# Performance work log

Measured on AMD Instinct MI355X. Metric: run time of the kernel, lower is better.

The kernel has to match this reference:

```python
import jax, jax.numpy as jnp
import numpy as np

G, N_NODES, E, H, D, IN_DIM, NS = 1024, 64, 128, 8, 32, 256, 48
EPS = 1e-6

def setup_inputs() -> dict:
    key = jax.random.key(0)
    ks = jax.random.split(key, 10)
    s = 1.0 / np.sqrt(IN_DIM)
    return {
        'h': jax.random.normal(ks[0], (G * N_NODES, IN_DIM), jnp.float32),
        'Wq': jax.random.normal(ks[1], (IN_DIM, H * D), jnp.float32) * s,
        'bq': jax.random.normal(ks[2], (H * D,), jnp.float32) * 0.01,
        'Wk': jax.random.normal(ks[3], (IN_DIM, H * D), jnp.float32) * s,
        'bk': jax.random.normal(ks[4], (H * D,), jnp.float32) * 0.01,
        'Wv': jax.random.normal(ks[5], (IN_DIM, H * D), jnp.float32) * s,
        'bv': jax.random.normal(ks[6], (H * D,), jnp.float32) * 0.01,
        'src': jax.random.randint(ks[7], (E,), 0, N_NODES, jnp.int32),
        'dst': jax.random.randint(ks[8], (E,), 0, N_NODES, jnp.int32),
        'ns': jax.random.randint(ks[9], (E, NS), 0, N_NODES, jnp.int32),
    }

def reference(h, Wq, bq, Wk, bk, Wv, bv, src, dst, ns):
    # per-node projections, reshaped per-graph: [G, n, H, D]
    Q = (h @ Wq + bq).reshape(G, N_NODES, H, D)
    K = (h @ Wk + bk).reshape(G, N_NODES, H, D)
    V = (h @ Wv + bv).reshape(G, N_NODES, H, D)
    # QK[g, s, h, t] = Q[g,s,h] . K[g,t,h], clamped as in torch .clamp(-5, 5)
    QK = jnp.clip(jnp.einsum('gshd,gthd->gsht', Q, K), -5.0, 5.0)  # [G, n, H, n]
    QKs = QK[:, src]  # rows for each edge's source node: [G, E, H, n]
    # numerator: QK[:, src_e, :, dst_e]
    num = jnp.take_along_axis(
        QKs, jnp.broadcast_to(dst[None, :, None, None].astype(jnp.int32), (G, E, H, 1)), axis=3
    )[..., 0]  # [G, E, H]
    # denominator: sum of QK[:, src_e, :, non_siblings(e)]
    den = jnp.take_along_axis(
        QKs, jnp.broadcast_to(ns[None, :, None, :], (G, E, H, NS)), axis=3
    ).sum(-1)  # [G, E, H]
    score = num / (den + EPS)  # [G, E, H]
    # scatter-sum aggregation: wV[g, dst] += V[g, src] * score; z[g, dst] += score
    msg = V[:, src] * score[..., None]  # [G, E, H, D]
    seg = (jnp.arange(G, dtype=jnp.int32)[:, None] * N_NODES + dst[None, :]).reshape(-1)
    wV = jax.ops.segment_sum(msg.reshape(G * E, H, D), seg, num_segments=G * N_NODES)
    z = jax.ops.segment_sum(score.reshape(G * E, H), seg, num_segments=G * N_NODES)
    return wV / (z[..., None] + EPS)  # [G*n, H, D]
```

## Files before the change

kernel.cpp:

```cpp
#include <hip/hip_runtime.h>

#define NG    1024
#define NN    64
#define NE    128
#define NH    8
#define ND    32
#define INDIM 256
#define NS_   48
#define EPS_  1e-6
#define BK    16

#define GBM   128
#define GBN   64
#define GBK   64

#define WS_QKV_FLOATS ((size_t)NG * NH * 3 * NN * ND)
#define WS_ELIST_OFF  (WS_QKV_FLOATS * sizeof(float))
#define WS_CNT_OFF    (WS_ELIST_OFF + (size_t)NN * 64 * sizeof(unsigned short))
#define WS_NEED2      (WS_CNT_OFF + (size_t)NN * sizeof(int))

typedef _Float16 half8_t __attribute__((ext_vector_type(8)));
typedef _Float16 half4_t __attribute__((ext_vector_type(4)));
typedef float    f32x4_t __attribute__((ext_vector_type(4)));

__device__ __forceinline__ void async_ld16(const float* gp, float* lp) {
  __builtin_amdgcn_global_load_lds(
      (const __attribute__((address_space(1))) void*)gp,
      (__attribute__((address_space(3))) void*)lp, 16, 0, 0);
}

__global__ __launch_bounds__(256, 2) void qkv_gemm_kernel(
    const float* __restrict__ h,
    const float* __restrict__ Wq, const float* __restrict__ bq,
    const float* __restrict__ Wk, const float* __restrict__ bk,
    float* __restrict__ ws)
{
  const int b    = blockIdx.x;
  const int xcd  = b & 7;
  const int slot = b >> 3;
  const int rt   = xcd * 128 + (slot >> 2);
  const int sel  = (slot >> 1) & 1;
  const int ct   = slot & 1;
  const int tid  = threadIdx.x;

  const float* W  = (sel == 0) ? Wq : Wk;
  const float* bs = (sel == 0) ? bq : bk;

  __shared__ __align__(16) float hT[2][64][16];
  __shared__ __align__(16) float wT[2][16][128];

  const int ty  = tid >> 5;
  const int tx  = tid & 31;
  const int r8  = ty * 8;
  const int ca  = tx * 4;

  const int wvid = tid >> 6;
  const int lane = tid & 63;

  float acc[8][4];
  #pragma unroll
  for (int i = 0; i < 8; ++i)
    #pragma unroll
    for (int j = 0; j < 4; ++j) acc[i][j] = 0.f;

  const float* gA = h + ((size_t)(rt * 64 + wvid * 16 + (lane >> 2))) * INDIM
                      + (lane & 3) * 4;
  const float* gB0 = W + ((size_t)(wvid * 4 + 0 + (lane >> 5))) * (NH * ND)
                       + ct * 128 + (lane & 31) * 4;
  const float* gB1 = W + ((size_t)(wvid * 4 + 2 + (lane >> 5))) * (NH * ND)
                       + ct * 128 + (lane & 31) * 4;
  float* lA[2]  = { &hT[0][wvid * 16][0], &hT[1][wvid * 16][0] };
  float* lB0[2] = { &wT[0][wvid * 4 + 0][0], &wT[1][wvid * 4 + 0][0] };
  float* lB1[2] = { &wT[0][wvid * 4 + 2][0], &wT[1][wvid * 4 + 2][0] };

  async_ld16(gA, lA[0]);
  async_ld16(gB0, lB0[0]);
  async_ld16(gB1, lB1[0]);

  for (int kc = 0; kc < INDIM / BK; ++kc) {
    __syncthreads();

    if (kc + 1 < INDIM / BK) {
      const int k0n = (kc + 1) * BK;
      const int nb  = (kc + 1) & 1;
      async_ld16(gA + k0n, lA[nb]);
      async_ld16(gB0 + (size_t)k0n * (NH * ND), lB0[nb]);
      async_ld16(gB1 + (size_t)k0n * (NH * ND), lB1[nb]);
    }

    const int cb = kc & 1;
    #pragma unroll
    for (int kg = 0; kg < 4; ++kg) {
      f32x4_t a4[8];
      #pragma unroll
      for (int i = 0; i < 8; ++i)
        a4[i] = *(const f32x4_t*)&hT[cb][r8 + i][kg * 4];
      f32x4_t b4[4];
      #pragma unroll
      for (int kk = 0; kk < 4; ++kk)
        b4[kk] = *(const f32x4_t*)&wT[cb][kg * 4 + kk][ca];

      #pragma unroll
      for (int kk = 0; kk < 4; ++kk) {
        const f32x4_t bb = b4[kk];
        #pragma unroll
        for (int i = 0; i < 8; ++i) {
          const float ai = a4[i][kk];
          acc[i][0] += ai * bb[0];
          acc[i][1] += ai * bb[1];
          acc[i][2] += ai * bb[2];
          acc[i][3] += ai * bb[3];
        }
      }
    }
  }

  const int col = ct * 128 + ca;
  const int hda = col >> 5, d0a = col & 31;
  float ba4[4];
  #pragma unroll
  for (int j = 0; j < 4; ++j) ba4[j] = bs[col + j];

  #pragma unroll
  for (int i = 0; i < 8; ++i) {
    const int r = rt * 64 + r8 + i;
    const int g = r >> 6, n = r & 63;
    float* opa = ws + ((((size_t)(g * NH + hda)) * 3 + sel) * NN + n) * ND + d0a;
    *(float4*)opa = make_float4(acc[i][0] + ba4[0], acc[i][1] + ba4[1],
                                acc[i][2] + ba4[2], acc[i][3] + ba4[3]);
  }
}

__device__ __forceinline__ void* swz_pt(void* base, int row, int k) {
  size_t byte = ((size_t)(row * GBK + k)) * 2;
  byte ^= (size_t)((row & 7) << 4);
  return (void*)((char*)base + byte);
}

__global__ __launch_bounds__(256, 2) void v_gemm_mfma(
    const float* __restrict__ h,
    const float* __restrict__ Wv, const float* __restrict__ bv,
    const int* __restrict__ dst,
    unsigned short* __restrict__ elist, int* __restrict__ cnt,
    float* __restrict__ ws)
{
  const int b = blockIdx.x;
  if (b >= 2048) {
    const int n = threadIdx.x;
    if (n < NN) {
      int c = 0;
      for (int e = 0; e < NE; ++e) {
        if (dst[e] == n) {
          if (c < 64) elist[n * 64 + c] = (unsigned short)e;
          ++c;
        }
      }
      cnt[n] = (c > 64) ? 64 : c;
    }
    return;
  }

  const int xcd  = b & 7;
  const int slot = b >> 3;
  const int rt   = xcd * 64 + (slot >> 2);
  const int ct   = slot & 3;

  __shared__ __align__(16) _Float16 Ahh[GBM * GBK];
  __shared__ __align__(16) _Float16 Ahl[GBM * GBK];
  __shared__ __align__(16) _Float16 Bhh[GBN * GBK];
  __shared__ __align__(16) _Float16 Bhl[GBN * GBK];

  const int tid  = threadIdx.x;
  const int lane = tid & 63;
  const int wvid = tid >> 6;
  const int wm   = wvid >> 1;
  const int wn   = wvid & 1;
  const int lr   = lane & 15;
  const int lg   = lane >> 4;

  f32x4_t acc0[4][2], acc1[4][2];
  #pragma unroll
  for (int i = 0; i < 4; ++i)
    #pragma unroll
    for (int j = 0; j < 2; ++j) {
      acc0[i][j] = (f32x4_t){0.f, 0.f, 0.f, 0.f};
      acc1[i][j] = (f32x4_t){0.f, 0.f, 0.f, 0.f};
    }

  const float* hA  = h + (size_t)rt * GBM * INDIM;
  const int bnn    = tid >> 2;
  const int bkh    = (tid & 3) * 16;
  const int c0     = ct * GBN;
  const float* wB  = Wv + (size_t)bkh * (NH * ND) + (c0 + bnn);

  for (int kc = 0; kc < INDIM / GBK; ++kc) {
    float4 av4[8];
    #pragma unroll
    for (int i = 0; i < 8; ++i) {
      const int idx = i * 256 + tid;
      const int row = idx >> 4, kq = idx & 15;
      av4[i] = *(const float4*)(hA + (size_t)row * INDIM + kc * GBK + kq * 4);
    }
    float wv16[16];
    #pragma unroll
    for (int j = 0; j < 16; ++j)
      wv16[j] = wB[(size_t)(kc * GBK + j) * (NH * ND)];

    if (kc) __syncthreads();

    #pragma unroll
    for (int i = 0; i < 8; ++i) {
      const int idx = i * 256 + tid;
      const int row = idx >> 4, kq = idx & 15;
      half4_t ph, pl;
      ph[0] = (_Float16)av4[i].x; ph[1] = (_Float16)av4[i].y;
      ph[2] = (_Float16)av4[i].z; ph[3] = (_Float16)av4[i].w;
      pl[0] = (_Float16)((av4[i].x - (float)ph[0]) * 2048.f);
      pl[1] = (_Float16)((av4[i].y - (float)ph[1]) * 2048.f);
      pl[2] = (_Float16)((av4[i].z - (float)ph[2]) * 2048.f);
      pl[3] = (_Float16)((av4[i].w - (float)ph[3]) * 2048.f);
      *(half4_t*)swz_pt(Ahh, row, kq * 4) = ph;
      *(half4_t*)swz_pt(Ahl, row, kq * 4) = pl;
    }
    #pragma unroll
    for (int c = 0; c < 2; ++c) {
      half8_t ph, pl;
      #pragma unroll
      for (int j = 0; j < 8; ++j) {
        const float a  = wv16[c * 8 + j];
        const _Float16 x = (_Float16)a;
        ph[j] = x;
        pl[j] = (_Float16)((a - (float)x) * 2048.f);
      }
      *(half8_t*)swz_pt(Bhh, bnn, bkh + c * 8) = ph;
      *(half8_t*)swz_pt(Bhl, bnn, bkh + c * 8) = pl;
    }
    __syncthreads();

    #pragma unroll
    for (int ks = 0; ks < 2; ++ks) {
      const int kb = ks * 32 + lg * 8;
      half8_t bh[2], bl[2];
      #pragma unroll
      for (int j = 0; j < 2; ++j) {
        const int colr = wn * 32 + j * 16 + lr;
        bh[j] = *(const half8_t*)swz_pt(Bhh, colr, kb);
        bl[j] = *(const half8_t*)swz_pt(Bhl, colr, kb);
      }
      #pragma unroll
      for (int i = 0; i < 4; ++i) {
        const int rowr = wm * 64 + i * 16 + lr;
        const half8_t ah = *(const half8_t*)swz_pt(Ahh, rowr, kb);
        const half8_t al = *(const half8_t*)swz_pt(Ahl, rowr, kb);
        #pragma unroll
        for (int j = 0; j < 2; ++j) {
          acc0[i][j] = __builtin_amdgcn_mfma_f32_16x16x32_f16(
              ah, bh[j], acc0[i][j], 0, 0, 0);
          acc1[i][j] = __builtin_amdgcn_mfma_f32_16x16x32_f16(
              ah, bl[j], acc1[i][j], 0, 0, 0);
          acc1[i][j] = __builtin_amdgcn_mfma_f32_16x16x32_f16(
              al, bh[j], acc1[i][j], 0, 0, 0);
        }
      }
    }
  }

  float bj[2];
  #pragma unroll
  for (int j = 0; j < 2; ++j) bj[j] = bv[c0 + wn * 32 + j * 16 + lr];

  #pragma unroll
  for (int i = 0; i < 4; ++i) {
    #pragma unroll
    for (int r = 0; r < 4; ++r) {
      const int R = rt * GBM + wm * 64 + i * 16 + lg * 4 + r;
      const int g = R >> 6, n = R & 63;
      #pragma unroll
      for (int j = 0; j < 2; ++j) {
        const int col = c0 + wn * 32 + j * 16 + lr;
        const int hd = col >> 5, d = col & 31;
        const float val = acc0[i][j][r] + acc1[i][j][r] * (1.0f / 2048.0f)
                          + bj[j];
        ws[((((size_t)(g * NH + hd)) * 3 + 2) * NN + n) * ND + d] = val;
      }
    }
  }
}

#define QSW(k, c) ((c) ^ ((((k) >> 3) & 3) << 2))

__global__ __launch_bounds__(256, 5) void attn_kernel(
    const float* __restrict__ ws,
    const int* __restrict__ src, const int* __restrict__ dst,
    const int* __restrict__ ns,
    const unsigned short* __restrict__ elist_g, const int* __restrict__ cnt_g,
    float* __restrict__ out, const int g0)
{
  const int hd  = blockIdx.x;
  const int g   = g0 + blockIdx.y;
  const int tid = threadIdx.x;
  const int ty  = tid >> 4, tx = tid & 15;

  __shared__ union {
    struct { float QT[32][68]; float KT[32][68]; } a;
    float QK[64][65];
  } uQ;
  __shared__ float Vs[64][36];
  __shared__ float  score_s[NE];
  __shared__ int    srcs[NE];
  __shared__ double z_s[NN];

  const float* base = ws + ((size_t)(g * NH + hd)) * 3 * (NN * ND);
  {
    const int nr = tid >> 3;
    const int d4 = (tid & 7) * 4;
    #pragma unroll
    for (int half = 0; half < 2; ++half) {
      const int n = half * 32 + nr;
      float4 q = *(const float4*)(base + (size_t)n * ND + d4);
      float4 k = *(const float4*)(base + (size_t)(NN * ND) + (size_t)n * ND + d4);
      float4 v = *(const float4*)(base + (size_t)(2 * NN * ND) + (size_t)n * ND + d4);
      uQ.a.QT[d4 + 0][QSW(d4 + 0, n)] = q.x;
      uQ.a.QT[d4 + 1][QSW(d4 + 1, n)] = q.y;
      uQ.a.QT[d4 + 2][QSW(d4 + 2, n)] = q.z;
      uQ.a.QT[d4 + 3][QSW(d4 + 3, n)] = q.w;
      uQ.a.KT[d4 + 0][QSW(d4 + 0, n)] = k.x;
      uQ.a.KT[d4 + 1][QSW(d4 + 1, n)] = k.y;
      uQ.a.KT[d4 + 2][QSW(d4 + 2, n)] = k.z;
      uQ.a.KT[d4 + 3][QSW(d4 + 3, n)] = k.w;
      *(float4*)&Vs[n][d4] = v;
    }
  }
  __syncthreads();

  {
    const int s0 = ty * 4, t0 = tx * 4;
    float qk[4][4];
    #pragma unroll
    for (int i = 0; i < 4; ++i)
      #pragma unroll
      for (int j = 0; j < 4; ++j) qk[i][j] = 0.f;
    #pragma unroll
    for (int k = 0; k < ND; ++k) {
      float4 qa = *(const float4*)&uQ.a.QT[k][QSW(k, s0)];
      float4 kb = *(const float4*)&uQ.a.KT[k][QSW(k, t0)];
      qk[0][0] += qa.x * kb.x; qk[0][1] += qa.x * kb.y; qk[0][2] += qa.x * kb.z; qk[0][3] += qa.x * kb.w;
      qk[1][0] += qa.y * kb.x; qk[1][1] += qa.y * kb.y; qk[1][2] += qa.y * kb.z; qk[1][3] += qa.y * kb.w;
      qk[2][0] += qa.z * kb.x; qk[2][1] += qa.z * kb.y; qk[2][2] += qa.z * kb.z; qk[2][3] += qa.z * kb.w;
      qk[3][0] += qa.w * kb.x; qk[3][1] += qa.w * kb.y; qk[3][2] += qa.w * kb.z; qk[3][3] += qa.w * kb.w;
    }
    __syncthreads();
    #pragma unroll
    for (int i = 0; i < 4; ++i)
      #pragma unroll
      for (int j = 0; j < 4; ++j) {
        float v = qk[i][j];
        v = fminf(5.f, fmaxf(-5.f, v));
        uQ.QK[s0 + i][t0 + j] = v;
      }
  }
  __syncthreads();

  if (tid < NE) {
    const int e = tid;
    const int s = src[e];
    srcs[e] = s;
    const float num = uQ.QK[s][dst[e]];
    double den = 0.0;
    const int* np_ = ns + (size_t)e * NS_;
    #pragma unroll
    for (int j = 0; j < NS_; ++j) den += (double)uQ.QK[s][np_[j]];
    score_s[e] = (float)((double)num / (den + (double)EPS_));
  }
  __syncthreads();

  if (tid < NN) {
    const int cn = cnt_g[tid];
    double zz = 0.0;
    for (int c = 0; c < cn; ++c)
      zz += (double)score_s[elist_g[tid * 64 + c]];
    z_s[tid] = zz;
  }
  __syncthreads();

  {
    const int n  = tid >> 2;
    const int d0 = (tid & 3) * 8;
    float wvv[8];
    #pragma unroll
    for (int i = 0; i < 8; ++i) wvv[i] = 0.f;
    const int cn = cnt_g[n];
    for (int c = 0; c < cn; ++c) {
      const int e  = elist_g[n * 64 + c];
      const float sc = score_s[e];
      const int s  = srcs[e];
      float4 v0 = *(const float4*)&Vs[s][d0];
      float4 v1 = *(const float4*)&Vs[s][d0 + 4];
      wvv[0] += sc * v0.x; wvv[1] += sc * v0.y; wvv[2] += sc * v0.z; wvv[3] += sc * v0.w;
      wvv[4] += sc * v1.x; wvv[5] += sc * v1.y; wvv[6] += sc * v1.z; wvv[7] += sc * v1.w;
    }
    const double zz = z_s[n] + (double)EPS_;
    float o[8];
    #pragma unroll
    for (int i = 0; i < 8; ++i) o[i] = (float)((double)wvv[i] / zz);
    float* op = out + (((size_t)(g * NN + n)) * NH + hd) * ND + d0;
    *(float4*)(op)     = make_float4(o[0], o[1], o[2], o[3]);
    *(float4*)(op + 4) = make_float4(o[4], o[5], o[6], o[7]);
  }
}

__global__ __launch_bounds__(256, 4) void raal_fused_kernel(
    const float* __restrict__ h,
    const float* __restrict__ Wq, const float* __restrict__ bq,
    const float* __restrict__ Wk, const float* __restrict__ bk,
    const float* __restrict__ Wv, const float* __restrict__ bv,
    const int*   __restrict__ src, const int* __restrict__ dst,
    const int*   __restrict__ ns,
    float* __restrict__ out)
{
  const int hd  = blockIdx.x;
  const int g   = blockIdx.y;
  const int tid = threadIdx.x;
  const int ty  = tid >> 4, tx = tid & 15;

  __shared__ union {
    struct { float QT[32][64]; float KT[32][64]; } s2;
    float QK[64][64];
  } uQ;
  __shared__ float Vs[64][32];
  __shared__ union {
    struct { float hT[BK][68]; float wT[BK][100]; } s1;
    struct { float score[NE]; int srcs[NE]; int dsts[NE];
             double z[NN]; unsigned short elist[NN][64]; int cnt[NN]; } s3;
  } uA;

  const int r0 = ty * 4;
  const int c4 = tx * 4;
  const int cv = tx * 2;

  float accqk[4][4], accv[4][2];
  #pragma unroll
  for (int i = 0; i < 4; ++i) {
    #pragma unroll
    for (int j = 0; j < 4; ++j) accqk[i][j] = 0.f;
    accv[i][0] = 0.f; accv[i][1] = 0.f;
  }

  const int lr  = tid >> 2;
  const int lk4 = (tid & 3) * 4;
  const int wr  = ty;
  const int wc  = tx * 2;
  const float* hrow = h + ((size_t)(g * NN + lr)) * INDIM + lk4;
  const size_t wcol = (size_t)hd * ND + wc;

  float4 hv; float2 wq2, wk2, wv2;
  {
    hv  = *(const float4*)(hrow);
    const size_t wro = (size_t)wr * (NH * ND) + wcol;
    wq2 = *(const float2*)(Wq + wro);
    wk2 = *(const float2*)(Wk + wro);
    wv2 = *(const float2*)(Wv + wro);
  }

  for (int kc = 0; kc < INDIM / BK; ++kc) {
    __syncthreads();
    uA.s1.hT[lk4 + 0][lr] = hv.x;
    uA.s1.hT[lk4 + 1][lr] = hv.y;
    uA.s1.hT[lk4 + 2][lr] = hv.z;
    uA.s1.hT[lk4 + 3][lr] = hv.w;
    *(float2*)&uA.s1.wT[wr][ 0 + wc] = wq2;
    *(float2*)&uA.s1.wT[wr][32 + wc] = wk2;
    *(float2*)&uA.s1.wT[wr][64 + wc] = wv2;
    __syncthreads();

    if (kc + 1 < INDIM / BK) {
      const int k0n = (kc + 1) * BK;
      hv  = *(const float4*)(hrow + k0n);
      const size_t wro = (size_t)(k0n + wr) * (NH * ND) + wcol;
      wq2 = *(const float2*)(Wq + wro);
      wk2 = *(const float2*)(Wk + wro);
      wv2 = *(const float2*)(Wv + wro);
    }

    #pragma unroll
    for (int k = 0; k < BK; ++k) {
      float4 a  = *(const float4*)&uA.s1.hT[k][r0];
      float4 b  = *(const float4*)&uA.s1.wT[k][c4];
      float2 bv2 = *(const float2*)&uA.s1.wT[k][64 + cv];
      #pragma unroll
      for (int i = 0; i < 4; ++i) {
        const float ai = (i == 0) ? a.x : (i == 1) ? a.y : (i == 2) ? a.z : a.w;
        accqk[i][0] += ai * b.x;
        accqk[i][1] += ai * b.y;
        accqk[i][2] += ai * b.z;
        accqk[i][3] += ai * b.w;
        accv[i][0]  += ai * bv2.x;
        accv[i][1]  += ai * bv2.y;
      }
    }
  }

  {
    if (tx < 8) {
      #pragma unroll
      for (int j = 0; j < 4; ++j) {
        const int c = c4 + j;
        const float b = bq[hd * ND + c];
        #pragma unroll
        for (int i = 0; i < 4; ++i) uQ.s2.QT[c][r0 + i] = accqk[i][j] + b;
      }
    } else {
      #pragma unroll
      for (int j = 0; j < 4; ++j) {
        const int c = c4 - 32 + j;
        const float b = bk[hd * ND + c];
        #pragma unroll
        for (int i = 0; i < 4; ++i) uQ.s2.KT[c][r0 + i] = accqk[i][j] + b;
      }
    }
    const float b0 = bv[hd * ND + cv], b1 = bv[hd * ND + cv + 1];
    #pragma unroll
    for (int i = 0; i < 4; ++i) {
      Vs[r0 + i][cv]     = accv[i][0] + b0;
      Vs[r0 + i][cv + 1] = accv[i][1] + b1;
    }
  }
  __syncthreads();

  {
    const int s0 = ty * 4, t0 = tx * 4;
    float qk[4][4];
    #pragma unroll
    for (int i = 0; i < 4; ++i)
      #pragma unroll
      for (int j = 0; j < 4; ++j) qk[i][j] = 0.f;
    #pragma unroll
    for (int k = 0; k < ND; ++k) {
      float4 qa = *(const float4*)&uQ.s2.QT[k][s0];
      float4 kb = *(const float4*)&uQ.s2.KT[k][t0];
      qk[0][0] += qa.x * kb.x; qk[0][1] += qa.x * kb.y; qk[0][2] += qa.x * kb.z; qk[0][3] += qa.x * kb.w;
      qk[1][0] += qa.y * kb.x; qk[1][1] += qa.y * kb.y; qk[1][2] += qa.y * kb.z; qk[1][3] += qa.y * kb.w;
      qk[2][0] += qa.z * kb.x; qk[2][1] += qa.z * kb.y; qk[2][2] += qa.z * kb.z; qk[2][3] += qa.z * kb.w;
      qk[3][0] += qa.w * kb.x; qk[3][1] += qa.w * kb.y; qk[3][2] += qa.w * kb.z; qk[3][3] += qa.w * kb.w;
    }
    __syncthreads();
    #pragma unroll
    for (int i = 0; i < 4; ++i)
      #pragma unroll
      for (int j = 0; j < 4; ++j) {
        float v = qk[i][j];
        v = fminf(5.f, fmaxf(-5.f, v));
        uQ.QK[s0 + i][t0 + j] = v;
      }
  }
  __syncthreads();

  if (tid < NE) {
    const int e = tid;
    const int s = src[e], dd = dst[e];
    uA.s3.srcs[e] = s; uA.s3.dsts[e] = dd;
    const float num = uQ.QK[s][dd];
    double den = 0.0;
    const int* np_ = ns + (size_t)e * NS_;
    #pragma unroll
    for (int j = 0; j < NS_; ++j) den += (double)uQ.QK[s][np_[j]];
    uA.s3.score[e] = (float)((double)num / (den + (double)EPS_));
  }
  __syncthreads();

  if (tid < NN) {
    int c = 0; double zz = 0.0;
    for (int e = 0; e < NE; ++e) {
      if (uA.s3.dsts[e] == tid) {
        zz += (double)uA.s3.score[e];
        if (c < 64) uA.s3.elist[tid][c] = (unsigned short)e;
        ++c;
      }
    }
    uA.s3.cnt[tid] = (c > 64) ? 64 : c;
    uA.s3.z[tid]   = zz;
  }
  __syncthreads();

  {
    const int n  = tid >> 2;
    const int d0 = (tid & 3) * 8;
    float wvv[8];
    #pragma unroll
    for (int i = 0; i < 8; ++i) wvv[i] = 0.f;
    const int cn = uA.s3.cnt[n];
    for (int c = 0; c < cn; ++c) {
      const int e  = uA.s3.elist[n][c];
      const float sc = uA.s3.score[e];
      const int s  = uA.s3.srcs[e];
      float4 v0 = *(const float4*)&Vs[s][d0];
      float4 v1 = *(const float4*)&Vs[s][d0 + 4];
      wvv[0] += sc * v0.x; wvv[1] += sc * v0.y; wvv[2] += sc * v0.z; wvv[3] += sc * v0.w;
      wvv[4] += sc * v1.x; wvv[5] += sc * v1.y; wvv[6] += sc * v1.z; wvv[7] += sc * v1.w;
    }
    const double zz = uA.s3.z[n] + (double)EPS_;
    float o[8];
    #pragma unroll
    for (int i = 0; i < 8; ++i) o[i] = (float)((double)wvv[i] / zz);
    float* op = out + (((size_t)(g * NN + n)) * NH + hd) * ND + d0;
    *(float4*)(op)     = make_float4(o[0], o[1], o[2], o[3]);
    *(float4*)(op + 4) = make_float4(o[4], o[5], o[6], o[7]);
  }
}

extern "C" void kernel_launch(void* const* d_in, const int* in_sizes, int n_in,
                              void* d_out, int out_size, void* d_ws, size_t ws_size,
                              hipStream_t stream) {
  const float* h   = (const float*)d_in[0];
  const float* Wq  = (const float*)d_in[1];
  const float* bq  = (const float*)d_in[2];
  const float* Wk  = (const float*)d_in[3];
  const float* bk  = (const float*)d_in[4];
  const float* Wv  = (const float*)d_in[5];
  const float* bv  = (const float*)d_in[6];
  const int*   src = (const int*)d_in[7];
  const int*   dst = (const int*)d_in[8];
  const int*   ns  = (const int*)d_in[9];
  float* out = (float*)d_out;

  dim3 b(256, 1, 1);
  if (ws_size >= WS_NEED2) {
    float* ws = (float*)d_ws;
    unsigned short* elist = (unsigned short*)((char*)d_ws + WS_ELIST_OFF);
    int* cnt = (int*)((char*)d_ws + WS_CNT_OFF);

    hipLaunchKernelGGL(qkv_gemm_kernel, dim3(4096, 1, 1), b, 0, stream,
                       h, Wq, bq, Wk, bk, ws);
    hipLaunchKernelGGL(v_gemm_mfma, dim3(2049, 1, 1), b, 0, stream,
                       h, Wv, bv, dst, elist, cnt, ws);
    hipLaunchKernelGGL(attn_kernel, dim3(NH, NG / 2, 1), b, 0, stream,
                       ws, src, dst, ns, elist, cnt, out, 0);
    hipLaunchKernelGGL(attn_kernel, dim3(NH, NG / 2, 1), b, 0, stream,
                       ws, src, dst, ns, elist, cnt, out, NG / 2);
  } else {
    hipLaunchKernelGGL(raal_fused_kernel, dim3(NH, NG, 1), b, 0, stream,
                       h, Wq, bq, Wk, bk, Wv, bv, src, dst, ns, out);
  }
}
```

Measured before the change: 461.7 us.

## Merge QK and V projection GEMMs into one launch and single attention launch

Combines the FP32 Q/K projection kernel and the split-FP16 MFMA V projection kernel into one grid, interleaving two QK blocks with one V block per triple and sharing LDS through a union. The two half-grid attention launches are collapsed into one full-grid launch. This removes launch overhead and the tail gaps between kernels, and lets the compute-heavy MFMA blocks overlap with the FMA-based blocks. The cost is register and LDS pressure set by the larger of the two paths, which may lower occupancy for the QK blocks.

```diff
diff --git a/kernel.cpp b/kernel.cpp
--- a/kernel.cpp
+++ b/kernel.cpp
@@ -29,124 +29,32 @@
       (__attribute__((address_space(3))) void*)lp, 16, 0, 0);
 }
 
-__global__ __launch_bounds__(256, 2) void qkv_gemm_kernel(
-    const float* __restrict__ h,
-    const float* __restrict__ Wq, const float* __restrict__ bq,
-    const float* __restrict__ Wk, const float* __restrict__ bk,
-    float* __restrict__ ws)
-{
-  const int b    = blockIdx.x;
-  const int xcd  = b & 7;
-  const int slot = b >> 3;
-  const int rt   = xcd * 128 + (slot >> 2);
-  const int sel  = (slot >> 1) & 1;
-  const int ct   = slot & 1;
-  const int tid  = threadIdx.x;
-
-  const float* W  = (sel == 0) ? Wq : Wk;
-  const float* bs = (sel == 0) ? bq : bk;
-
-  __shared__ __align__(16) float hT[2][64][16];
-  __shared__ __align__(16) float wT[2][16][128];
-
-  const int ty  = tid >> 5;
-  const int tx  = tid & 31;
-  const int r8  = ty * 8;
-  const int ca  = tx * 4;
-
-  const int wvid = tid >> 6;
-  const int lane = tid & 63;
-
-  float acc[8][4];
-  #pragma unroll
-  for (int i = 0; i < 8; ++i)
-    #pragma unroll
-    for (int j = 0; j < 4; ++j) acc[i][j] = 0.f;
-
-  const float* gA = h + ((size_t)(rt * 64 + wvid * 16 + (lane >> 2))) * INDIM
-                      + (lane & 3) * 4;
-  const float* gB0 = W + ((size_t)(wvid * 4 + 0 + (lane >> 5))) * (NH * ND)
-                       + ct * 128 + (lane & 31) * 4;
-  const float* gB1 = W + ((size_t)(wvid * 4 + 2 + (lane >> 5))) * (NH * ND)
-                       + ct * 128 + (lane & 31) * 4;
-  float* lA[2]  = { &hT[0][wvid * 16][0], &hT[1][wvid * 16][0] };
-  float* lB0[2] = { &wT[0][wvid * 4 + 0][0], &wT[1][wvid * 4 + 0][0] };
-  float* lB1[2] = { &wT[0][wvid * 4 + 2][0], &wT[1][wvid * 4 + 2][0] };
-
-  async_ld16(gA, lA[0]);
-  async_ld16(gB0, lB0[0]);
-  async_ld16(gB1, lB1[0]);
-
-  for (int kc = 0; kc < INDIM / BK; ++kc) {
-    __syncthreads();
-
-    if (kc + 1 < INDIM / BK) {
-      const int k0n = (kc + 1) * BK;
-      const int nb  = (kc + 1) & 1;
-      async_ld16(gA + k0n, lA[nb]);
-      async_ld16(gB0 + (size_t)k0n * (NH * ND), lB0[nb]);
-      async_ld16(gB1 + (size_t)k0n * (NH * ND), lB1[nb]);
-    }
-
-    const int cb = kc & 1;
-    #pragma unroll
-    for (int kg = 0; kg < 4; ++kg) {
-      f32x4_t a4[8];
-      #pragma unroll
-      for (int i = 0; i < 8; ++i)
-        a4[i] = *(const f32x4_t*)&hT[cb][r8 + i][kg * 4];
-      f32x4_t b4[4];
-      #pragma unroll
-      for (int kk = 0; kk < 4; ++kk)
-        b4[kk] = *(const f32x4_t*)&wT[cb][kg * 4 + kk][ca];
-
-      #pragma unroll
-      for (int kk = 0; kk < 4; ++kk) {
-        const f32x4_t bb = b4[kk];
-        #pragma unroll
-        for (int i = 0; i < 8; ++i) {
-          const float ai = a4[i][kk];
-          acc[i][0] += ai * bb[0];
-          acc[i][1] += ai * bb[1];
-          acc[i][2] += ai * bb[2];
-          acc[i][3] += ai * bb[3];
-        }
-      }
-    }
-  }
-
-  const int col = ct * 128 + ca;
-  const int hda = col >> 5, d0a = col & 31;
-  float ba4[4];
-  #pragma unroll
-  for (int j = 0; j < 4; ++j) ba4[j] = bs[col + j];
-
-  #pragma unroll
-  for (int i = 0; i < 8; ++i) {
-    const int r = rt * 64 + r8 + i;
-    const int g = r >> 6, n = r & 63;
-    float* opa = ws + ((((size_t)(g * NH + hda)) * 3 + sel) * NN + n) * ND + d0a;
-    *(float4*)opa = make_float4(acc[i][0] + ba4[0], acc[i][1] + ba4[1],
-                                acc[i][2] + ba4[2], acc[i][3] + ba4[3]);
-  }
-}
-
 __device__ __forceinline__ void* swz_pt(void* base, int row, int k) {
   size_t byte = ((size_t)(row * GBK + k)) * 2;
   byte ^= (size_t)((row & 7) << 4);
   return (void*)((char*)base + byte);
 }
 
-__global__ __launch_bounds__(256, 2) void v_gemm_mfma(
+__global__ __launch_bounds__(256, 2) void qkv_v_fused_kernel(
     const float* __restrict__ h,
+    const float* __restrict__ Wq, const float* __restrict__ bq,
+    const float* __restrict__ Wk, const float* __restrict__ bk,
     const float* __restrict__ Wv, const float* __restrict__ bv,
     const int* __restrict__ dst,
     unsigned short* __restrict__ elist, int* __restrict__ cnt,
     float* __restrict__ ws)
 {
-  const int b = blockIdx.x;
-  if (b >= 2048) {
-    const int n = threadIdx.x;
+  __shared__ __align__(16) union {
+    struct { float hT[2][64][16]; float wT[2][16][128]; } qk;
+    struct { _Float16 Ahh[GBM * GBK]; _Float16 Ahl[GBM * GBK];
+             _Float16 Bhh[GBN * GBK]; _Float16 Bhl[GBN * GBK]; } v;
+  } sm;
+
+  const int bid = blockIdx.x;
+  const int tid = threadIdx.x;
+
+  if (bid >= 6144) {
+    const int n = tid;
     if (n < NN) {
       int c = 0;
       for (int e = 0; e < NE; ++e) {
@@ -160,128 +68,216 @@
     return;
   }
 
-  const int xcd  = b & 7;
-  const int slot = b >> 3;
-  const int rt   = xcd * 64 + (slot >> 2);
-  const int ct   = slot & 3;
-
-  __shared__ __align__(16) _Float16 Ahh[GBM * GBK];
-  __shared__ __align__(16) _Float16 Ahl[GBM * GBK];
-  __shared__ __align__(16) _Float16 Bhh[GBN * GBK];
-  __shared__ __align__(16) _Float16 Bhl[GBN * GBK];
-
-  const int tid  = threadIdx.x;
+  const int trip = bid / 3;
+  const int rr   = bid % 3;
+  const int wvid = tid >> 6;
   const int lane = tid & 63;
-  const int wvid = tid >> 6;
-  const int wm   = wvid >> 1;
-  const int wn   = wvid & 1;
-  const int lr   = lane & 15;
-  const int lg   = lane >> 4;
-
-  f32x4_t acc0[4][2], acc1[4][2];
-  #pragma unroll
-  for (int i = 0; i < 4; ++i)
-    #pragma unroll
-    for (int j = 0; j < 2; ++j) {
-      acc0[i][j] = (f32x4_t){0.f, 0.f, 0.f, 0.f};
-      acc1[i][j] = (f32x4_t){0.f, 0.f, 0.f, 0.f};
-    }
-
-  const float* hA  = h + (size_t)rt * GBM * INDIM;
-  const int bnn    = tid >> 2;
-  const int bkh    = (tid & 3) * 16;
-  const int c0     = ct * GBN;
-  const float* wB  = Wv + (size_t)bkh * (NH * ND) + (c0 + bnn);
-
-  for (int kc = 0; kc < INDIM / GBK; ++kc) {
-    float4 av4[8];
+
+  if (rr < 2) {
+    const int b    = trip * 2 + rr;
+    const int xcd  = b & 7;
+    const int slot = b >> 3;
+    const int rt   = xcd * 128 + (slot >> 2);
+    const int sel  = (slot >> 1) & 1;
+    const int ct   = slot & 1;
+
+    const float* W  = (sel == 0) ? Wq : Wk;
+    const float* bs = (sel == 0) ? bq : bk;
+
+    const int ty  = tid >> 5;
+    const int tx  = tid & 31;
+    const int r8  = ty * 8;
+    const int ca  = tx * 4;
+
+    float acc[8][4];
+    #pragma unroll
+    for (int i = 0; i < 8; ++i)
+      #pragma unroll
+      for (int j = 0; j < 4; ++j) acc[i][j] = 0.f;
+
+    const float* gA = h + ((size_t)(rt * 64 + wvid * 16 + (lane >> 2))) * INDIM
+                        + (lane & 3) * 4;
+    const float* gB0 = W + ((size_t)(wvid * 4 + 0 + (lane >> 5))) * (NH * ND)
+                         + ct * 128 + (lane & 31) * 4;
+    const float* gB1 = W + ((size_t)(wvid * 4 + 2 + (lane >> 5))) * (NH * ND)
+                         + ct * 128 + (lane & 31) * 4;
+    float* lA[2]  = { &sm.qk.hT[0][wvid * 16][0], &sm.qk.hT[1][wvid * 16][0] };
+    float* lB0[2] = { &sm.qk.wT[0][wvid * 4 + 0][0], &sm.qk.wT[1][wvid * 4 + 0][0] };
+    float* lB1[2] = { &sm.qk.wT[0][wvid * 4 + 2][0], &sm.qk.wT[1][wvid * 4 + 2][0] };
+
+    async_ld16(gA, lA[0]);
+    async_ld16(gB0, lB0[0]);
+    async_ld16(gB1, lB1[0]);
+
+    for (int kc = 0; kc < INDIM / BK; ++kc) {
+      __syncthreads();
+
+      if (kc + 1 < INDIM / BK) {
+        const int k0n = (kc + 1) * BK;
+        const int nb  = (kc + 1) & 1;
+        async_ld16(gA + k0n, lA[nb]);
+        async_ld16(gB0 + (size_t)k0n * (NH * ND), lB0[nb]);
+        async_ld16(gB1 + (size_t)k0n * (NH * ND), lB1[nb]);
+      }
+
+      const int cb = kc & 1;
+      #pragma unroll
+      for (int kg = 0; kg < 4; ++kg) {
+        f32x4_t a4[8];
+        #pragma unroll
+        for (int i = 0; i < 8; ++i)
+          a4[i] = *(const f32x4_t*)&sm.qk.hT[cb][r8 + i][kg * 4];
+        f32x4_t b4[4];
+        #pragma unroll
+        for (int kk = 0; kk < 4; ++kk)
+          b4[kk] = *(const f32x4_t*)&sm.qk.wT[cb][kg * 4 + kk][ca];
+
+        #pragma unroll
+        for (int kk = 0; kk < 4; ++kk) {
+          const f32x4_t bb = b4[kk];
+          #pragma unroll
+          for (int i = 0; i < 8; ++i) {
+            const float ai = a4[i][kk];
+            acc[i][0] = __builtin_fmaf(ai, bb[0], acc[i][0]);
+            acc[i][1] = __builtin_fmaf(ai, bb[1], acc[i][1]);
+            acc[i][2] = __builtin_fmaf(ai, bb[2], acc[i][2]);
+            acc[i][3] = __builtin_fmaf(ai, bb[3], acc[i][3]);
+          }
+        }
+      }
+    }
+
+    const int col = ct * 128 + ca;
+    const int hda = col >> 5, d0a = col & 31;
+    float ba4[4];
+    #pragma unroll
+    for (int j = 0; j < 4; ++j) ba4[j] = bs[col + j];
+
     #pragma unroll
     for (int i = 0; i < 8; ++i) {
-      const int idx = i * 256 + tid;
-      const int row = idx >> 4, kq = idx & 15;
-      av4[i] = *(const float4*)(hA + (size_t)row * INDIM + kc * GBK + kq * 4);
-    }
-    float wv16[16];
-    #pragma unroll
-    for (int j = 0; j < 16; ++j)
-      wv16[j] = wB[(size_t)(kc * GBK + j) * (NH * ND)];
-
-    if (kc) __syncthreads();
-
-    #pragma unroll
-    for (int i = 0; i < 8; ++i) {
-      const int idx = i * 256 + tid;
-      const int row = idx >> 4, kq = idx & 15;
-      half4_t ph, pl;
-      ph[0] = (_Float16)av4[i].x; ph[1] = (_Float16)av4[i].y;
-      ph[2] = (_Float16)av4[i].z; ph[3] = (_Float16)av4[i].w;
-      pl[0] = (_Float16)((av4[i].x - (float)ph[0]) * 2048.f);
-      pl[1] = (_Float16)((av4[i].y - (float)ph[1]) * 2048.f);
-      pl[2] = (_Float16)((av4[i].z - (float)ph[2]) * 2048.f);
-      pl[3] = (_Float16)((av4[i].w - (float)ph[3]) * 2048.f);
-      *(half4_t*)swz_pt(Ahh, row, kq * 4) = ph;
-      *(half4_t*)swz_pt(Ahl, row, kq * 4) = pl;
-    }
-    #pragma unroll
-    for (int c = 0; c < 2; ++c) {
-      half8_t ph, pl;
-      #pragma unroll
-      for (int j = 0; j < 8; ++j) {
-        const float a  = wv16[c * 8 + j];
-        const _Float16 x = (_Float16)a;
-        ph[j] = x;
-        pl[j] = (_Float16)((a - (float)x) * 2048.f);
-      }
-      *(half8_t*)swz_pt(Bhh, bnn, bkh + c * 8) = ph;
-      *(half8_t*)swz_pt(Bhl, bnn, bkh + c * 8) = pl;
-    }
-    __syncthreads();
-
-    #pragma unroll
-    for (int ks = 0; ks < 2; ++ks) {
-      const int kb = ks * 32 + lg * 8;
-      half8_t bh[2], bl[2];
+      const int r = rt * 64 + r8 + i;
+      const int g = r >> 6, n = r & 63;
+      float* opa = ws + ((((size_t)(g * NH + hda)) * 3 + sel) * NN + n) * ND + d0a;
+      *(float4*)opa = make_float4(acc[i][0] + ba4[0], acc[i][1] + ba4[1],
+                                  acc[i][2] + ba4[2], acc[i][3] + ba4[3]);
+    }
+  } else {
+    const int vb   = trip;
+    const int xcd  = vb & 7;
+    const int slot = vb >> 3;
+    const int rt   = xcd * 64 + (slot >> 2);
+    const int ct   = slot & 3;
+
+    const int wm   = wvid >> 1;
+    const int wn   = wvid & 1;
+    const int lr   = lane & 15;
+    const int lg   = lane >> 4;
+
+    f32x4_t acc0[4][2], acc1[4][2];
+    #pragma unroll
+    for (int i = 0; i < 4; ++i)
       #pragma unroll
       for (int j = 0; j < 2; ++j) {
-        const int colr = wn * 32 + j * 16 + lr;
-        bh[j] = *(const half8_t*)swz_pt(Bhh, colr, kb);
-        bl[j] = *(const half8_t*)swz_pt(Bhl, colr, kb);
-      }
-      #pragma unroll
-      for (int i = 0; i < 4; ++i) {
-        const int rowr = wm * 64 + i * 16 + lr;
-        const half8_t ah = *(const half8_t*)swz_pt(Ahh, rowr, kb);
-        const half8_t al = *(const half8_t*)swz_pt(Ahl, rowr, kb);
+        acc0[i][j] = (f32x4_t){0.f, 0.f, 0.f, 0.f};
+        acc1[i][j] = (f32x4_t){0.f, 0.f, 0.f, 0.f};
+      }
+
+    const float* hA  = h + (size_t)rt * GBM * INDIM;
+    const int bnn    = tid >> 2;
+    const int bkh    = (tid & 3) * 16;
+    const int c0     = ct * GBN;
+    const float* wB  = Wv + (size_t)bkh * (NH * ND) + (c0 + bnn);
+
+    for (int kc = 0; kc < INDIM / GBK; ++kc) {
+      float4 av4[8];
+      #pragma unroll
+      for (int i = 0; i < 8; ++i) {
+        const int idx = i * 256 + tid;
+        const int row = idx >> 4, kq = idx & 15;
+        av4[i] = *(const float4*)(hA + (size_t)row * INDIM + kc * GBK + kq * 4);
+      }
+      float wv16[16];
+      #pragma unroll
+      for (int j = 0; j < 16; ++j)
+        wv16[j] = wB[(size_t)(kc * GBK + j) * (NH * ND)];
+
+      if (kc) __syncthreads();
+
+      #pragma unroll
+      for (int i = 0; i < 8; ++i) {
+        const int idx = i * 256 + tid;
+        const int row = idx >> 4, kq = idx & 15;
+        half4_t ph, pl;
+        ph[0] = (_Float16)av4[i].x; ph[1] = (_Float16)av4[i].y;
+        ph[2] = (_Float16)av4[i].z; ph[3] = (_Float16)av4[i].w;
+        pl[0] = (_Float16)((av4[i].x - (float)ph[0]) * 2048.f);
+        pl[1] = (_Float16)((av4[i].y - (float)ph[1]) * 2048.f);
+        pl[2] = (_Float16)((av4[i].z - (float)ph[2]) * 2048.f);
+        pl[3] = (_Float16)((av4[i].w - (float)ph[3]) * 2048.f);
+        *(half4_t*)swz_pt(sm.v.Ahh, row, kq * 4) = ph;
+        *(half4_t*)swz_pt(sm.v.Ahl, row, kq * 4) = pl;
+      }
+      #pragma unroll
+      for (int c = 0; c < 2; ++c) {
+        half8_t ph, pl;
+        #pragma unroll
+        for (int j = 0; j < 8; ++j) {
+          const float a  = wv16[c * 8 + j];
+          const _Float16 x = (_Float16)a;
+          ph[j] = x;
+          pl[j] = (_Float16)((a - (float)x) * 2048.f);
+        }
+        *(half8_t*)swz_pt(sm.v.Bhh, bnn, bkh + c * 8) = ph;
+        *(half8_t*)swz_pt(sm.v.Bhl, bnn, bkh + c * 8) = pl;
+      }
+      __syncthreads();
+
+      #pragma unroll
+      for (int ks = 0; ks < 2; ++ks) {
+        const int kb = ks * 32 + lg * 8;
+        half8_t bh[2], bl[2];
         #pragma unroll
         for (int j = 0; j < 2; ++j) {
-          acc0[i][j] = __builtin_amdgcn_mfma_f32_16x16x32_f16(
-              ah, bh[j], acc0[i][j], 0, 0, 0);
-          acc1[i][j] = __builtin_amdgcn_mfma_f32_16x16x32_f16(
-              ah, bl[j], acc1[i][j], 0, 0, 0);
-          acc1[i][j] = __builtin_amdgcn_mfma_f32_16x16x32_f16(
-              al, bh[j], acc1[i][j], 0, 0, 0);
+          const int colr = wn * 32 + j * 16 + lr;
+          bh[j] = *(const half8_t*)swz_pt(sm.v.Bhh, colr, kb);
+          bl[j] = *(const half8_t*)swz_pt(sm.v.Bhl, colr, kb);
         }
-      }
-    }
-  }
-
-  float bj[2];
-  #pragma unroll
-  for (int j = 0; j < 2; ++j) bj[j] = bv[c0 + wn * 32 + j * 16 + lr];
-
-  #pragma unroll
-  for (int i = 0; i < 4; ++i) {
-    #pragma unroll
-    for (int r = 0; r < 4; ++r) {
-      const int R = rt * GBM + wm * 64 + i * 16 + lg * 4 + r;
-      const int g = R >> 6, n = R & 63;
-      #pragma unroll
-      for (int j = 0; j < 2; ++j) {
-        const int col = c0 + wn * 32 + j * 16 + lr;
-        const int hd = col >> 5, d = col & 31;
-        const float val = acc0[i][j][r] + acc1[i][j][r] * (1.0f / 2048.0f)
-                          + bj[j];
-        ws[((((size_t)(g * NH + hd)) * 3 + 2) * NN + n) * ND + d] = val;
+        #pragma unroll
+        for (int i = 0; i < 4; ++i) {
+          const int rowr = wm * 64 + i * 16 + lr;
+          const half8_t ah = *(const half8_t*)swz_pt(sm.v.Ahh, rowr, kb);
+          const half8_t al = *(const half8_t*)swz_pt(sm.v.Ahl, rowr, kb);
+          #pragma unroll
+          for (int j = 0; j < 2; ++j) {
+            acc0[i][j] = __builtin_amdgcn_mfma_f32_16x16x32_f16(
+                ah, bh[j], acc0[i][j], 0, 0, 0);
+            acc1[i][j] = __builtin_amdgcn_mfma_f32_16x16x32_f16(
+                ah, bl[j], acc1[i][j], 0, 0, 0);
+            acc1[i][j] = __builtin_amdgcn_mfma_f32_16x16x32_f16(
+                al, bh[j], acc1[i][j], 0, 0, 0);
+          }
+        }
+      }
+    }
+
+    float bj[2];
+    #pragma unroll
+    for (int j = 0; j < 2; ++j) bj[j] = bv[c0 + wn * 32 + j * 16 + lr];
+
+    #pragma unroll
+    for (int i = 0; i < 4; ++i) {
+      #pragma unroll
+      for (int r = 0; r < 4; ++r) {
+        const int R = rt * GBM + wm * 64 + i * 16 + lg * 4 + r;
+        const int g = R >> 6, n = R & 63;
+        #pragma unroll
+        for (int j = 0; j < 2; ++j) {
+          const int col = c0 + wn * 32 + j * 16 + lr;
+          const int hd = col >> 5, d = col & 31;
+          const float val = acc0[i][j][r] + acc1[i][j][r] * (1.0f / 2048.0f)
+                            + bj[j];
+          ws[((((size_t)(g * NH + hd)) * 3 + 2) * NN + n) * ND + d] = val;
+        }
       }
     }
   }
@@ -294,10 +290,10 @@
     const int* __restrict__ src, const int* __restrict__ dst,
     const int* __restrict__ ns,
     const unsigned short* __restrict__ elist_g, const int* __restrict__ cnt_g,
-    float* __restrict__ out, const int g0)
+    float* __restrict__ out)
 {
   const int hd  = blockIdx.x;
-  const int g   = g0 + blockIdx.y;
+  const int g   = blockIdx.y;
   const int tid = threadIdx.x;
   const int ty  = tid >> 4, tx = tid & 15;
 
@@ -629,14 +625,10 @@
     unsigned short* elist = (unsigned short*)((char*)d_ws + WS_ELIST_OFF);
     int* cnt = (int*)((char*)d_ws + WS_CNT_OFF);
 
-    hipLaunchKernelGGL(qkv_gemm_kernel, dim3(4096, 1, 1), b, 0, stream,
-                       h, Wq, bq, Wk, bk, ws);
-    hipLaunchKernelGGL(v_gemm_mfma, dim3(2049, 1, 1), b, 0, stream,
-                       h, Wv, bv, dst, elist, cnt, ws);
-    hipLaunchKernelGGL(attn_kernel, dim3(NH, NG / 2, 1), b, 0, stream,
-                       ws, src, dst, ns, elist, cnt, out, 0);
-    hipLaunchKernelGGL(attn_kernel, dim3(NH, NG / 2, 1), b, 0, stream,
-                       ws, src, dst, ns, elist, cnt, out, NG / 2);
+    hipLaunchKernelGGL(qkv_v_fused_kernel, dim3(6145, 1, 1), b, 0, stream,
+                       h, Wq, bq, Wk, bk, Wv, bv, dst, elist, cnt, ws);
+    hipLaunchKernelGGL(attn_kernel, dim3(NH, NG, 1), b, 0, stream,
+                       ws, src, dst, ns, elist, cnt, out);
   } else {
     hipLaunchKernelGGL(raal_fused_kernel, dim3(NH, NG, 1), b, 0, stream,
                        h, Wq, bq, Wk, bk, Wv, bv, src, dst, ns, out);
```

Result: slower. 474.1 us (+2.7%).

## Fuse V projection GEMM into attention kernel and split edge setup

Applied to the files above, without the earlier changes.

Removes the standalone V GEMM kernel and computes each graph-head's 64x32 V tile inside the attention kernel with split-fp16 MFMA, writing it straight to shared memory. This avoids writing V to the workspace and reading it back, and merges the two attention half-launches into a single grid. Edge-list construction moves to its own tiny kernel. The cost is that each block now re-reads its graph's h rows (all 8 head blocks read the same h), occupancy drops from 5 to 4 blocks per CU, and the small per-block GEMM gets little reuse.

```diff
diff --git a/kernel.cpp b/kernel.cpp
--- a/kernel.cpp
+++ b/kernel.cpp
@@ -9,10 +9,6 @@
 #define NS_   48
 #define EPS_  1e-6
 #define BK    16
-
-#define GBM   128
-#define GBN   64
-#define GBK   64
 
 #define WS_QKV_FLOATS ((size_t)NG * NH * 3 * NN * ND)
 #define WS_ELIST_OFF  (WS_QKV_FLOATS * sizeof(float))
@@ -131,184 +127,127 @@
   }
 }
 
-__device__ __forceinline__ void* swz_pt(void* base, int row, int k) {
-  size_t byte = ((size_t)(row * GBK + k)) * 2;
-  byte ^= (size_t)((row & 7) << 4);
-  return (void*)((char*)base + byte);
+__global__ void edge_setup_kernel(const int* __restrict__ dst,
+                                  unsigned short* __restrict__ elist,
+                                  int* __restrict__ cnt)
+{
+  const int n = threadIdx.x;
+  if (n < NN) {
+    int c = 0;
+    for (int e = 0; e < NE; ++e) {
+      if (dst[e] == n) {
+        if (c < 64) elist[n * 64 + c] = (unsigned short)e;
+        ++c;
+      }
+    }
+    cnt[n] = (c > 64) ? 64 : c;
+  }
 }
 
-__global__ __launch_bounds__(256, 2) void v_gemm_mfma(
+#define QSW(k, c) ((c) ^ ((((k) >> 3) & 3) << 2))
+
+__global__ __launch_bounds__(256, 4) void attn_kernel(
     const float* __restrict__ h,
     const float* __restrict__ Wv, const float* __restrict__ bv,
-    const int* __restrict__ dst,
-    unsigned short* __restrict__ elist, int* __restrict__ cnt,
-    float* __restrict__ ws)
-{
-  const int b = blockIdx.x;
-  if (b >= 2048) {
-    const int n = threadIdx.x;
-    if (n < NN) {
-      int c = 0;
-      for (int e = 0; e < NE; ++e) {
-        if (dst[e] == n) {
-          if (c < 64) elist[n * 64 + c] = (unsigned short)e;
-          ++c;
-        }
-      }
-      cnt[n] = (c > 64) ? 64 : c;
-    }
-    return;
-  }
-
-  const int xcd  = b & 7;
-  const int slot = b >> 3;
-  const int rt   = xcd * 64 + (slot >> 2);
-  const int ct   = slot & 3;
-
-  __shared__ __align__(16) _Float16 Ahh[GBM * GBK];
-  __shared__ __align__(16) _Float16 Ahl[GBM * GBK];
-  __shared__ __align__(16) _Float16 Bhh[GBN * GBK];
-  __shared__ __align__(16) _Float16 Bhl[GBN * GBK];
-
-  const int tid  = threadIdx.x;
-  const int lane = tid & 63;
-  const int wvid = tid >> 6;
-  const int wm   = wvid >> 1;
-  const int wn   = wvid & 1;
-  const int lr   = lane & 15;
-  const int lg   = lane >> 4;
-
-  f32x4_t acc0[4][2], acc1[4][2];
-  #pragma unroll
-  for (int i = 0; i < 4; ++i)
-    #pragma unroll
-    for (int j = 0; j < 2; ++j) {
-      acc0[i][j] = (f32x4_t){0.f, 0.f, 0.f, 0.f};
-      acc1[i][j] = (f32x4_t){0.f, 0.f, 0.f, 0.f};
-    }
-
-  const float* hA  = h + (size_t)rt * GBM * INDIM;
-  const int bnn    = tid >> 2;
-  const int bkh    = (tid & 3) * 16;
-  const int c0     = ct * GBN;
-  const float* wB  = Wv + (size_t)bkh * (NH * ND) + (c0 + bnn);
-
-  for (int kc = 0; kc < INDIM / GBK; ++kc) {
-    float4 av4[8];
-    #pragma unroll
-    for (int i = 0; i < 8; ++i) {
-      const int idx = i * 256 + tid;
-      const int row = idx >> 4, kq = idx & 15;
-      av4[i] = *(const float4*)(hA + (size_t)row * INDIM + kc * GBK + kq * 4);
-    }
-    float wv16[16];
-    #pragma unroll
-    for (int j = 0; j < 16; ++j)
-      wv16[j] = wB[(size_t)(kc * GBK + j) * (NH * ND)];
-
-    if (kc) __syncthreads();
-
-    #pragma unroll
-    for (int i = 0; i < 8; ++i) {
-      const int idx = i * 256 + tid;
-      const int row = idx >> 4, kq = idx & 15;
-      half4_t ph, pl;
-      ph[0] = (_Float16)av4[i].x; ph[1] = (_Float16)av4[i].y;
-      ph[2] = (_Float16)av4[i].z; ph[3] = (_Float16)av4[i].w;
-      pl[0] = (_Float16)((av4[i].x - (float)ph[0]) * 2048.f);
-      pl[1] = (_Float16)((av4[i].y - (float)ph[1]) * 2048.f);
-      pl[2] = (_Float16)((av4[i].z - (float)ph[2]) * 2048.f);
-      pl[3] = (_Float16)((av4[i].w - (float)ph[3]) * 2048.f);
-      *(half4_t*)swz_pt(Ahh, row, kq * 4) = ph;
-      *(half4_t*)swz_pt(Ahl, row, kq * 4) = pl;
-    }
-    #pragma unroll
-    for (int c = 0; c < 2; ++c) {
-      half8_t ph, pl;
-      #pragma unroll
-      for (int j = 0; j < 8; ++j) {
-        const float a  = wv16[c * 8 + j];
-        const _Float16 x = (_Float16)a;
-        ph[j] = x;
-        pl[j] = (_Float16)((a - (float)x) * 2048.f);
-      }
-      *(half8_t*)swz_pt(Bhh, bnn, bkh + c * 8) = ph;
-      *(half8_t*)swz_pt(Bhl, bnn, bkh + c * 8) = pl;
-    }
-    __syncthreads();
-
-    #pragma unroll
-    for (int ks = 0; ks < 2; ++ks) {
-      const int kb = ks * 32 + lg * 8;
-      half8_t bh[2], bl[2];
-      #pragma unroll
-      for (int j = 0; j < 2; ++j) {
-        const int colr = wn * 32 + j * 16 + lr;
-        bh[j] = *(const half8_t*)swz_pt(Bhh, colr, kb);
-        bl[j] = *(const half8_t*)swz_pt(Bhl, colr, kb);
-      }
-      #pragma unroll
-      for (int i = 0; i < 4; ++i) {
-        const int rowr = wm * 64 + i * 16 + lr;
-        const half8_t ah = *(const half8_t*)swz_pt(Ahh, rowr, kb);
-        const half8_t al = *(const half8_t*)swz_pt(Ahl, rowr, kb);
-        #pragma unroll
-        for (int j = 0; j < 2; ++j) {
-          acc0[i][j] = __builtin_amdgcn_mfma_f32_16x16x32_f16(
-              ah, bh[j], acc0[i][j], 0, 0, 0);
-          acc1[i][j] = __builtin_amdgcn_mfma_f32_16x16x32_f16(
-              ah, bl[j], acc1[i][j], 0, 0, 0);
-          acc1[i][j] = __builtin_amdgcn_mfma_f32_16x16x32_f16(
-              al, bh[j], acc1[i][j], 0, 0, 0);
-        }
-      }
-    }
-  }
-
-  float bj[2];
-  #pragma unroll
-  for (int j = 0; j < 2; ++j) bj[j] = bv[c0 + wn * 32 + j * 16 + lr];
-
-  #pragma unroll
-  for (int i = 0; i < 4; ++i) {
-    #pragma unroll
-    for (int r = 0; r < 4; ++r) {
-      const int R = rt * GBM + wm * 64 + i * 16 + lg * 4 + r;
-      const int g = R >> 6, n = R & 63;
-      #pragma unroll
-      for (int j = 0; j < 2; ++j) {
-        const int col = c0 + wn * 32 + j * 16 + lr;
-        const int hd = col >> 5, d = col & 31;
-        const float val = acc0[i][j][r] + acc1[i][j][r] * (1.0f / 2048.0f)
-                          + bj[j];
-        ws[((((size_t)(g * NH + hd)) * 3 + 2) * NN + n) * ND + d] = val;
-      }
-    }
-  }
-}
-
-#define QSW(k, c) ((c) ^ ((((k) >> 3) & 3) << 2))
-
-__global__ __launch_bounds__(256, 5) void attn_kernel(
     const float* __restrict__ ws,
     const int* __restrict__ src, const int* __restrict__ dst,
     const int* __restrict__ ns,
     const unsigned short* __restrict__ elist_g, const int* __restrict__ cnt_g,
-    float* __restrict__ out, const int g0)
+    float* __restrict__ out)
 {
   const int hd  = blockIdx.x;
-  const int g   = g0 + blockIdx.y;
+  const int g   = blockIdx.y;
   const int tid = threadIdx.x;
   const int ty  = tid >> 4, tx = tid & 15;
-
-  __shared__ union {
+  const int lane = tid & 63;
+  const int wvid = tid >> 6;
+  const int lr   = lane & 15;
+  const int lg   = lane >> 4;
+
+  __shared__ __align__(16) union {
     struct { float QT[32][68]; float KT[32][68]; } a;
     float QK[64][65];
+    struct { _Float16 Ah[64][40]; _Float16 Al[64][40];
+             _Float16 Bh[32][40]; _Float16 Bl[32][40]; } v;
   } uQ;
-  __shared__ float Vs[64][36];
+  __shared__ float  Vs[64][36];
   __shared__ float  score_s[NE];
   __shared__ int    srcs[NE];
   __shared__ double z_s[NN];
+
+  {
+    f32x4_t vacc0[2], vacc1[2];
+    #pragma unroll
+    for (int j = 0; j < 2; ++j) {
+      vacc0[j] = (f32x4_t){0.f, 0.f, 0.f, 0.f};
+      vacc1[j] = (f32x4_t){0.f, 0.f, 0.f, 0.f};
+    }
+    const float* hg = h + (size_t)(g * NN) * INDIM;
+    const int hr = tid >> 2;
+    const int hk = (tid & 3) * 8;
+    const int wc_ = tid & 31;
+    const int wq  = (tid >> 5) * 4;
+
+    for (int kc = 0; kc < 8; ++kc) {
+      float4 h0 = *(const float4*)(hg + (size_t)hr * INDIM + kc * 32 + hk);
+      float4 h1 = *(const float4*)(hg + (size_t)hr * INDIM + kc * 32 + hk + 4);
+      float wv4[4];
+      #pragma unroll
+      for (int j = 0; j < 4; ++j)
+        wv4[j] = Wv[(size_t)(kc * 32 + wq + j) * (NH * ND) + hd * ND + wc_];
+
+      if (kc) __syncthreads();
+
+      {
+        half8_t ph, pl;
+        const float hv[8] = {h0.x, h0.y, h0.z, h0.w, h1.x, h1.y, h1.z, h1.w};
+        #pragma unroll
+        for (int j = 0; j < 8; ++j) {
+          const _Float16 x = (_Float16)hv[j];
+          ph[j] = x;
+          pl[j] = (_Float16)((hv[j] - (float)x) * 2048.f);
+        }
+        *(half8_t*)&uQ.v.Ah[hr][hk] = ph;
+        *(half8_t*)&uQ.v.Al[hr][hk] = pl;
+      }
+      {
+        half4_t ph, pl;
+        #pragma unroll
+        for (int j = 0; j < 4; ++j) {
+          const _Float16 x = (_Float16)wv4[j];
+          ph[j] = x;
+          pl[j] = (_Float16)((wv4[j] - (float)x) * 2048.f);
+        }
+        *(half4_t*)&uQ.v.Bh[wc_][wq] = ph;
+        *(half4_t*)&uQ.v.Bl[wc_][wq] = pl;
+      }
+      __syncthreads();
+
+      const half8_t va_h = *(const half8_t*)&uQ.v.Ah[16 * wvid + lr][lg * 8];
+      const half8_t va_l = *(const half8_t*)&uQ.v.Al[16 * wvid + lr][lg * 8];
+      #pragma unroll
+      for (int j = 0; j < 2; ++j) {
+        const half8_t vb_h = *(const half8_t*)&uQ.v.Bh[j * 16 + lr][lg * 8];
+        const half8_t vb_l = *(const half8_t*)&uQ.v.Bl[j * 16 + lr][lg * 8];
+        vacc0[j] = __builtin_amdgcn_mfma_f32_16x16x32_f16(
+            va_h, vb_h, vacc0[j], 0, 0, 0);
+        vacc1[j] = __builtin_amdgcn_mfma_f32_16x16x32_f16(
+            va_h, vb_l, vacc1[j], 0, 0, 0);
+        vacc1[j] = __builtin_amdgcn_mfma_f32_16x16x32_f16(
+            va_l, vb_h, vacc1[j], 0, 0, 0);
+      }
+    }
+
+    #pragma unroll
+    for (int j = 0; j < 2; ++j) {
+      const float bvj = bv[hd * ND + j * 16 + lr];
+      #pragma unroll
+      for (int r = 0; r < 4; ++r)
+        Vs[16 * wvid + lg * 4 + r][j * 16 + lr] =
+            vacc0[j][r] + vacc1[j][r] * (1.0f / 2048.0f) + bvj;
+    }
+  }
+  __syncthreads();
 
   const float* base = ws + ((size_t)(g * NH + hd)) * 3 * (NN * ND);
   {
@@ -319,7 +258,6 @@
       const int n = half * 32 + nr;
       float4 q = *(const float4*)(base + (size_t)n * ND + d4);
       float4 k = *(const float4*)(base + (size_t)(NN * ND) + (size_t)n * ND + d4);
-      float4 v = *(const float4*)(base + (size_t)(2 * NN * ND) + (size_t)n * ND + d4);
       uQ.a.QT[d4 + 0][QSW(d4 + 0, n)] = q.x;
       uQ.a.QT[d4 + 1][QSW(d4 + 1, n)] = q.y;
       uQ.a.QT[d4 + 2][QSW(d4 + 2, n)] = q.z;
@@ -328,7 +266,6 @@
       uQ.a.KT[d4 + 1][QSW(d4 + 1, n)] = k.y;
       uQ.a.KT[d4 + 2][QSW(d4 + 2, n)] = k.z;
       uQ.a.KT[d4 + 3][QSW(d4 + 3, n)] = k.w;
-      *(float4*)&Vs[n][d4] = v;
     }
   }
   __syncthreads();
@@ -344,10 +281,22 @@
     for (int k = 0; k < ND; ++k) {
       float4 qa = *(const float4*)&uQ.a.QT[k][QSW(k, s0)];
       float4 kb = *(const float4*)&uQ.a.KT[k][QSW(k, t0)];
-      qk[0][0] += qa.x * kb.x; qk[0][1] += qa.x * kb.y; qk[0][2] += qa.x * kb.z; qk[0][3] += qa.x * kb.w;
-      qk[1][0] += qa.y * kb.x; qk[1][1] += qa.y * kb.y; qk[1][2] += qa.y * kb.z; qk[1][3] += qa.y * kb.w;
-      qk[2][0] += qa.z * kb.x; qk[2][1] += qa.z * kb.y; qk[2][2] += qa.z * kb.z; qk[2][3] += qa.z * kb.w;
-      qk[3][0] += qa.w * kb.x; qk[3][1] += qa.w * kb.y; qk[3][2] += qa.w * kb.z; qk[3][3] += qa.w * kb.w;
+      qk[0][0] = __builtin_fmaf(qa.x, kb.x, qk[0][0]);
+      qk[0][1] = __builtin_fmaf(qa.x, kb.y, qk[0][1]);
+      qk[0][2] = __builtin_fmaf(qa.x, kb.z, qk[0][2]);
+      qk[0][3] = __builtin_fmaf(qa.x, kb.w, qk[0][3]);
+      qk[1][0] = __builtin_fmaf(qa.y, kb.x, qk[1][0]);
+      qk[1][1] = __builtin_fmaf(qa.y, kb.y, qk[1][1]);
+      qk[1][2] = __builtin_fmaf(qa.y, kb.z, qk[1][2]);
+      qk[1][3] = __builtin_fmaf(qa.y, kb.w, qk[1][3]);
+      qk[2][0] = __builtin_fmaf(qa.z, kb.x, qk[2][0]);
+      qk[2][1] = __builtin_fmaf(qa.z, kb.y, qk[2][1]);
+      qk[2][2] = __builtin_fmaf(qa.z, kb.z, qk[2][2]);
+      qk[2][3] = __builtin_fmaf(qa.z, kb.w, qk[2][3]);
+      qk[3][0] = __builtin_fmaf(qa.w, kb.x, qk[3][0]);
+      qk[3][1] = __builtin_fmaf(qa.w, kb.y, qk[3][1]);
+      qk[3][2] = __builtin_fmaf(qa.w, kb.z, qk[3][2]);
+      qk[3][3] = __builtin_fmaf(qa.w, kb.w, qk[3][3]);
     }
     __syncthreads();
     #pragma unroll
@@ -631,12 +580,10 @@
 
     hipLaunchKernelGGL(qkv_gemm_kernel, dim3(4096, 1, 1), b, 0, stream,
                        h, Wq, bq, Wk, bk, ws);
-    hipLaunchKernelGGL(v_gemm_mfma, dim3(2049, 1, 1), b, 0, stream,
-                       h, Wv, bv, dst, elist, cnt, ws);
-    hipLaunchKernelGGL(attn_kernel, dim3(NH, NG / 2, 1), b, 0, stream,
-                       ws, src, dst, ns, elist, cnt, out, 0);
-    hipLaunchKernelGGL(attn_kernel, dim3(NH, NG / 2, 1), b, 0, stream,
-                       ws, src, dst, ns, elist, cnt, out, NG / 2);
+    hipLaunchKernelGGL(edge_setup_kernel, dim3(1, 1, 1), dim3(64, 1, 1), 0, stream,
+                       dst, elist, cnt);
+    hipLaunchKernelGGL(attn_kernel, dim3(NH, NG, 1), b, 0, stream,
+                       h, Wv, bv, ws, src, dst, ns, elist, cnt, out);
   } else {
     hipLaunchKernelGGL(raal_fused_kernel, dim3(NH, NG, 1), b, 0, stream,
                        h, Wq, bq, Wk, bk, Wv, bv, src, dst, ns, out);
```

Measured after the change: 458.0 us. No clear change (-0.8%).
